# Kernel tuning notes

Hardware: AMD Instinct MI355X
Metric: run time of the kernel (lower is better)

Reference implementation:

```python
import jax, jax.numpy as jnp
import numpy as np

T, B, C, H, W = 4, 8, 256, 56, 56
HEADS = 8
D_NORM = 8.0
LAMDA = 1
CV = C * LAMDA
EPS = 1e-5


def quant_if(x, D):
    # Q_IFNode with Quant surrogate: integer spike counts clip(round(x),0,D),
    # straight-through gradient = 1 on [0, D].
    y = jnp.clip(jnp.round(x), 0.0, D)
    mask = ((x >= 0.0) & (x <= D)).astype(x.dtype)
    return x * mask + jax.lax.stop_gradient(y - x * mask)


def conv_bn(x, w, p):
    # 1x1 conv (pointwise channel mix) fused with eval-mode BatchNorm.
    # x: [T,B,Cin,H,W], w: [Cout,Cin], p: [4,Cout]=(gamma,beta,mean,var)
    y = jnp.einsum('oc,tbchw->tbohw', w, x)
    gamma, beta, mean, var = p[0], p[1], p[2], p[3]
    s = gamma / jnp.sqrt(var + EPS)
    return y * s[None, None, :, None, None] + (beta - mean * s)[None, None, :, None, None]


def _to_heads(t, c):
    # [T,B,c,H,W] -> [T,B,HEADS,N,c//HEADS]  (channel split h-outer, matches torch reshape)
    return t.reshape(T, B, HEADS, c // HEADS, H * W).transpose(0, 1, 2, 4, 3)


def setup_inputs():
    key = jax.random.key(0)
    ks = jax.random.split(key, 9)

    def bn_params(k, c):
        k1, k2, k3, k4 = jax.random.split(k, 4)
        return jnp.stack([
            jax.random.uniform(k1, (c,)) + 0.5,        # gamma
            jax.random.normal(k2, (c,)) * 0.1,          # beta
            jax.random.normal(k3, (c,)) * 0.1,          # running mean
            jax.random.uniform(k4, (c,)) + 0.5,         # running var
        ]).astype(jnp.float32)

    x = jax.random.normal(ks[0], (T, B, C, H, W), dtype=jnp.float32)
    w_scale = 1.0 / np.sqrt(C)
    return {
        'x': x,
        'qw': jax.random.normal(ks[1], (C, C), dtype=jnp.float32) * w_scale,
        'qbn': bn_params(ks[2], C),
        'kw': jax.random.normal(ks[3], (C, C), dtype=jnp.float32) * w_scale,
        'kbn': bn_params(ks[4], C),
        'vw': jax.random.normal(ks[5], (CV, C), dtype=jnp.float32) * w_scale,
        'vbn': bn_params(ks[6], CV),
        'pw': jax.random.normal(ks[7], (C, CV), dtype=jnp.float32) * w_scale,
        'pbn': bn_params(ks[8], C),
    }


def reference(x, qw, qbn, kw, kbn, vw, vbn, pw, pbn):
    dh = C // HEADS
    scale = dh ** (-0.5)

    xs = quant_if(x, D_NORM) / D_NORM                       # head_spike / D_Norm
    q = conv_bn(xs, qw, qbn)
    k = conv_bn(xs, kw, kbn)
    v = conv_bn(xs, vw, vbn)

    qh = _to_heads(quant_if(q, D_NORM) / D_NORM, C)         # [T,B,h,N,dh]
    kh = _to_heads(quant_if(k, D_NORM) / D_NORM, C)
    vh = _to_heads(quant_if(v, D_NORM) / D_NORM, CV)        # [T,B,h,N,dv]

    # Softmax-free linear attention: (q @ k^T) @ v == q @ (k^T @ v), O(N*d^2).
    kv = jnp.einsum('tbhnd,tbhne->tbhde', kh, vh)            # [T,B,h,dh,dv]
    o = jnp.einsum('tbhnd,tbhde->tbhne', qh, kv) * (scale * 2.0)

    # [T,B,h,N,dv] -> [T,B,CV,N]
    o = o.transpose(0, 1, 2, 4, 3).reshape(T, B, CV, H * W)
    o = quant_if(o, D_NORM) / D_NORM                         # attn_spike / D_Norm
    o = o.reshape(T, B, CV, H, W)
    out = conv_bn(o, pw, pbn)                                # [T,B,C,H,W]
    return out
```

## Files before the change

### kernel.cpp

```cpp
#include <hip/hip_runtime.h>
#include <stdint.h>

#define TB_ 32
#define C_ 256
#define N_ 3136
#define TBC (C_ * N_)
#define ACT_SZ (TB_ * TBC)
#define XSB_TB 819200
#define PARTS 7
#define CHUNK 448

typedef __attribute__((ext_vector_type(8))) short bf16x8;
typedef __attribute__((ext_vector_type(4))) float f32x4;

__device__ __forceinline__ void glds16(const void* gp, void* lp) {
  __builtin_amdgcn_global_load_lds(
      (const __attribute__((address_space(1))) unsigned int*)gp,
      (__attribute__((address_space(3))) unsigned int*)lp, 16, 0, 0);
}

__device__ __forceinline__ unsigned short bf16rn(float f, float* val) {
  unsigned b = __float_as_uint(f);
  unsigned r = (b + 0x7fffu + ((b >> 16) & 1u)) >> 16;
  *val = __uint_as_float(r << 16);
  return (unsigned short)r;
}

__device__ __forceinline__ int dot4u(unsigned a, unsigned b, int c) {
  c += (int)(a & 255u)         * (int)(b & 255u);
  c += (int)((a >> 8) & 255u)  * (int)((b >> 8) & 255u);
  c += (int)((a >> 16) & 255u) * (int)((b >> 16) & 255u);
  c += (int)(a >> 24)          * (int)(b >> 24);
  return c;
}

__device__ __forceinline__ int dot4(unsigned a, unsigned b, int c) {
#if defined(__has_builtin)
#if __has_builtin(__builtin_amdgcn_sdot4)
  return __builtin_amdgcn_sdot4((int)a, (int)b, c, false);
#else
  return dot4u(a, b, c);
#endif
#else
  return dot4u(a, b, c);
#endif
}

__global__ __launch_bounds__(256) void prep_all(
    const float* __restrict__ qbn, const float* __restrict__ kbn,
    const float* __restrict__ vbn, const float* __restrict__ pbn,
    const float* __restrict__ qw, const float* __restrict__ kw,
    const float* __restrict__ vw, const float* __restrict__ pw,
    float* __restrict__ bnw, unsigned short* __restrict__ wsp,
    int* __restrict__ kvg) {
  const int bx = blockIdx.x;
  const int t = threadIdx.x;
  if (bx == 0) {
    const float* ps[4] = {qbn, kbn, vbn, pbn};
#pragma unroll
    for (int i = 0; i < 4; ++i) {
      const float* p = ps[i];
      float g = p[t], be = p[256 + t], mn = p[512 + t], vr = p[768 + t];
      float s = g / sqrtf(vr + 1e-5f);
      float b = __fsub_rn(be, __fmul_rn(mn, s));
      bnw[i * 512 + t] = s;
      bnw[i * 512 + 256 + t] = b;
    }
  } else if (bx <= 1024) {
    const float* Ws[4] = {qw, kw, vw, pw};
    int id = bx - 1, co = id & 255, m = id >> 8;
    float w = Ws[m][co * 256 + t];
    float h1, h2, h3r;
    unsigned short u1 = bf16rn(w, &h1);
    float r1 = __fsub_rn(w, h1);
    unsigned short u2 = bf16rn(r1, &h2);
    float r2 = __fsub_rn(r1, h2);
    unsigned short u3 = bf16rn(r2, &h3r);
    int rt = co >> 7, ks = t >> 5;
    int lane = (co & 15) + 16 * ((t >> 3) & 3);
    unsigned short us[3] = {u1, u2, u3};
#pragma unroll
    for (int sp = 0; sp < 3; ++sp) {
      size_t off = (size_t)((((m * 3 + sp) * 2 + rt) * 8 + ks)) * 4096 + lane * 8 + (t & 7);
      wsp[off] = us[sp];
    }
  } else {
    int tb = bx - 1025;
    int4* p = (int4*)(kvg + (size_t)tb * 8192);
    for (int i = t; i < 2048; i += 256) p[i] = make_int4(0, 0, 0, 0);
  }
}

__global__ __launch_bounds__(256) void quant_x_t(const float* __restrict__ x,
                                                 unsigned short* __restrict__ xsb) {
  __shared__ unsigned short s[64 * 68];
  const int t = threadIdx.x;
  const int n0 = blockIdx.x * 64;
  const int tb = blockIdx.y;
  const float* X = x + (size_t)tb * TBC;
  const int nl = t & 63, cq = t >> 6;
  const int c16 = t >> 4, p4 = (t & 15) * 4;

  unsigned short* dstb = xsb + (size_t)tb * XSB_TB;
  for (int cb = 0; cb < 4; ++cb) {
    int cbase = cb * 64;
#pragma unroll
    for (int i = 0; i < 4; ++i) {
      int c = i * 16 + c16;
      float4 v = *(const float4*)&X[(size_t)(cbase + c) * N_ + n0 + p4];
      unsigned short r0 = (unsigned short)(__float_as_uint(fminf(fmaxf(rintf(v.x), 0.f), 8.f)) >> 16);
      unsigned short r1 = (unsigned short)(__float_as_uint(fminf(fmaxf(rintf(v.y), 0.f), 8.f)) >> 16);
      unsigned short r2 = (unsigned short)(__float_as_uint(fminf(fmaxf(rintf(v.z), 0.f), 8.f)) >> 16);
      unsigned short r3 = (unsigned short)(__float_as_uint(fminf(fmaxf(rintf(v.w), 0.f), 8.f)) >> 16);
      uint2 pk2;
      pk2.x = (unsigned)r0 | ((unsigned)r1 << 16);
      pk2.y = (unsigned)r2 | ((unsigned)r3 << 16);
      *(uint2*)&s[c * 68 + p4] = pk2;
    }
    __syncthreads();
#pragma unroll 2
    for (int j = 0; j < 2; ++j) {
      int ccl = j * 4 + cq;
      int cc = cb * 8 + ccl;
      unsigned short v8[8];
#pragma unroll
      for (int d = 0; d < 8; ++d) v8[d] = s[(ccl * 8 + d) * 68 + nl];
      int n = n0 + nl;
      uint4 pk;
      pk.x = (unsigned)v8[0] | ((unsigned)v8[1] << 16);
      pk.y = (unsigned)v8[2] | ((unsigned)v8[3] << 16);
      pk.z = (unsigned)v8[4] | ((unsigned)v8[5] << 16);
      pk.w = (unsigned)v8[6] | ((unsigned)v8[7] << 16);
      *(uint4*)&dstb[(size_t)(n >> 4) * 4096 + cc * 128 + (n & 15) * 8] = pk;
    }
    __syncthreads();
  }
}

__global__ __launch_bounds__(256) void qkv_mfma_sw(
    const unsigned short* __restrict__ xsb, const unsigned short* __restrict__ wsp,
    const float* __restrict__ bnw,
    uint8_t* __restrict__ qsb, uint8_t* __restrict__ ks_, uint8_t* __restrict__ vs) {
  __shared__ __align__(16) char smem[49152];
  const int t = threadIdx.x;
  const int L = t & 63, w = t >> 6;
  const int wrow = w >> 1, wcol = w & 1;
  const int b = blockIdx.x;
  const int oct = b / 48, rem = b % 48;
  const int s = rem >> 3, gl = rem & 7;
  const int g = oct * 8 + gl;
  const int ntile = g % 25, tb = g / 25;
  const int conv = s >> 1, rt = s & 1;
  const int n0 = ntile * 128;

  const char* Bb = (const char*)(xsb + (size_t)tb * XSB_TB) + (size_t)ntile * 65536;
  const char* Ab = (const char*)wsp + ((size_t)(conv * 3) * 16 + rt * 8) * 8192;

  f32x4 acc[4][4];
#pragma unroll
  for (int i = 0; i < 4; ++i)
#pragma unroll
    for (int j = 0; j < 4; ++j) acc[i][j] = (f32x4){0.f, 0.f, 0.f, 0.f};

  glds16(Ab + t * 16, smem + t * 16);
  glds16(Ab + t * 16 + 4096, smem + t * 16 + 4096);
  glds16(Bb + (size_t)w * 8192 + L * 16, smem + 8192 + t * 16);
  glds16(Bb + (size_t)(w + 4) * 8192 + L * 16, smem + 8192 + t * 16 + 4096);
  {
    char* slot1 = smem + 16384;
    const char* Ak1 = Ab + 8192;
    glds16(Ak1 + t * 16, slot1 + t * 16);
    glds16(Ak1 + t * 16 + 4096, slot1 + t * 16 + 4096);
    const char* Bk1 = Bb + 1024;
    glds16(Bk1 + (size_t)w * 8192 + L * 16, slot1 + 8192 + t * 16);
    glds16(Bk1 + (size_t)(w + 4) * 8192 + L * 16, slot1 + 8192 + t * 16 + 4096);
  }

#pragma unroll 1
  for (int st = 0; st < 24; ++st) {
    if (st < 23) {
      asm volatile("s_waitcnt vmcnt(4)" ::: "memory");
    } else {
      asm volatile("s_waitcnt vmcnt(0)" ::: "memory");
    }
    __builtin_amdgcn_s_barrier();
    const int s2 = st + 2;
    if (s2 < 24) {
      char* slotn = smem + (s2 % 3) * 16384;
      const char* Ak = Ab + (size_t)(((s2 >> 3) * 16) + (s2 & 7)) * 8192;
      glds16(Ak + t * 16, slotn + t * 16);
      glds16(Ak + t * 16 + 4096, slotn + t * 16 + 4096);
      const char* Bk = Bb + (size_t)(s2 & 7) * 1024;
      glds16(Bk + (size_t)w * 8192 + L * 16, slotn + 8192 + t * 16);
      glds16(Bk + (size_t)(w + 4) * 8192 + L * 16, slotn + 8192 + t * 16 + 4096);
    }
    char* slotc = smem + (st % 3) * 16384;
    bf16x8 af[4], bfr[4];
#pragma unroll
    for (int i = 0; i < 4; ++i) {
      af[i] = *(const bf16x8*)(slotc + (wrow * 4 + i) * 1024 + L * 16);
      bfr[i] = *(const bf16x8*)(slotc + 8192 + (wcol * 4 + i) * 1024 + L * 16);
    }
#pragma unroll
    for (int i = 0; i < 4; ++i)
#pragma unroll
      for (int j = 0; j < 4; ++j)
        acc[i][j] = __builtin_amdgcn_mfma_f32_16x16x32_bf16(af[i], bfr[j], acc[i][j], 0, 0, 0);
  }

  const float* sbn = bnw + conv * 512;
  const int rbase = rt * 128;
  if (conv == 0) {
    uint8_t* qtb = qsb + (size_t)tb * XSB_TB;
#pragma unroll
    for (int i = 0; i < 4; ++i) {
      int co0 = rbase + wrow * 64 + i * 16 + ((L >> 4) << 2);
      float s0 = sbn[co0], b0 = sbn[256 + co0];
      float s1 = sbn[co0 + 1], b1 = sbn[256 + co0 + 1];
      float s2v = sbn[co0 + 2], b2 = sbn[256 + co0 + 2];
      float s3 = sbn[co0 + 3], b3 = sbn[256 + co0 + 3];
#pragma unroll
      for (int j = 0; j < 4; ++j) {
        int n = n0 + wcol * 64 + j * 16 + (L & 15);
        if (n < N_) {
          float ss[4] = {s0, s1, s2v, s3}, bb[4] = {b0, b1, b2, b3};
          unsigned wb = 0;
#pragma unroll
          for (int r = 0; r < 4; ++r) {
            float y = acc[i][j][r] * 0.125f;
            float tt = __fadd_rn(__fmul_rn(y, ss[r]), bb[r]);
            float rr = fminf(fmaxf(rintf(tt), 0.f), 8.f);
            wb |= ((unsigned)(uint8_t)rr) << (8 * r);
          }
          *(unsigned*)&qtb[(size_t)(n >> 4) * 4096 + (co0 >> 3) * 128 + (n & 15) * 8 + (co0 & 7)] = wb;
        }
      }
    }
  } else {
    uint8_t* outp = (conv == 1 ? ks_ : vs) + (size_t)tb * TBC;
#pragma unroll
    for (int i = 0; i < 4; ++i) {
      int co0 = rbase + wrow * 64 + i * 16 + ((L >> 4) << 2);
#pragma unroll
      for (int j = 0; j < 4; ++j) {
        int n = n0 + wcol * 64 + j * 16 + (L & 15);
        if (n < N_) {
#pragma unroll
          for (int r = 0; r < 4; ++r) {
            int co = co0 + r;
            float y = acc[i][j][r] * 0.125f;
            float tt = __fadd_rn(__fmul_rn(y, sbn[co]), sbn[256 + co]);
            float rr = fminf(fmaxf(rintf(tt), 0.f), 8.f);
            outp[(size_t)co * N_ + n] = (uint8_t)rr;
          }
        }
      }
    }
  }
}

__global__ __launch_bounds__(256) void attn_kv(
    const uint8_t* __restrict__ ks, const uint8_t* __restrict__ vs,
    int* __restrict__ kvg) {
  const int h = blockIdx.x, tb = blockIdx.y, part = blockIdx.z;
  const int tid = threadIdx.x;
  __shared__ unsigned sk[32][68];
  __shared__ unsigned sv[32][68];
  const uint8_t* K = ks + (size_t)tb * TBC + h * 32 * N_;
  const uint8_t* V = vs + (size_t)tb * TBC + h * 32 * N_;
  const int d0 = (tid >> 4) * 2;
  const int e0 = (tid & 15) * 2;
  const int vsw = ((e0 >> 1) & 7) << 2;
  const int pbase = part * CHUNK;
  const int pend = pbase + CHUNK;
  int acc[2][2] = {};

  for (int nt = 0; nt < 2; ++nt) {
    int n0 = pbase + nt * 256;
    if (n0 >= pend) break;
    if (nt) __syncthreads();
#pragma unroll
    for (int i = 0; i < 8; ++i) {
      int idx = tid + i * 256;
      int d = idx >> 6, w2 = idx & 63;
      int n = n0 + w2 * 4;
      unsigned kw_ = 0, vw_ = 0;
      if (n < pend) {
        kw_ = *(const unsigned*)&K[d * N_ + n];
        vw_ = *(const unsigned*)&V[d * N_ + n];
      }
      sk[d][w2] = kw_;
      sv[d][w2 ^ (((d >> 1) & 7) << 2)] = vw_;
    }
    __syncthreads();
#pragma unroll
    for (int w2 = 0; w2 < 64; w2 += 4) {
      uint4 ka = *(const uint4*)&sk[d0][w2];
      uint4 kb = *(const uint4*)&sk[d0 + 1][w2];
      uint4 va = *(const uint4*)&sv[e0][w2 ^ vsw];
      uint4 vb = *(const uint4*)&sv[e0 + 1][w2 ^ vsw];
      unsigned kwds[2][4] = {{ka.x, ka.y, ka.z, ka.w}, {kb.x, kb.y, kb.z, kb.w}};
      unsigned vwds[2][4] = {{va.x, va.y, va.z, va.w}, {vb.x, vb.y, vb.z, vb.w}};
#pragma unroll
      for (int di = 0; di < 2; ++di)
#pragma unroll
        for (int ej = 0; ej < 2; ++ej)
#pragma unroll
          for (int c = 0; c < 4; ++c)
            acc[di][ej] = dot4(kwds[di][c], vwds[ej][c], acc[di][ej]);
    }
  }
  int* dst = kvg + ((size_t)(tb * 8 + h)) * 1024;
  atomicAdd(&dst[d0 * 32 + e0], acc[0][0]);
  atomicAdd(&dst[d0 * 32 + e0 + 1], acc[0][1]);
  atomicAdd(&dst[(d0 + 1) * 32 + e0], acc[1][0]);
  atomicAdd(&dst[(d0 + 1) * 32 + e0 + 1], acc[1][1]);
}

__global__ __launch_bounds__(256) void kv_finish(const int* __restrict__ kvg,
                                                 unsigned short* __restrict__ kvimg) {
  const int tb = blockIdx.x, t = threadIdx.x;
  const int* src = kvg + (size_t)tb * 8192;
  unsigned short* dst = kvimg + (size_t)tb * 24576;
#pragma unroll 4
  for (int i = 0; i < 32; ++i) {
    int idx = t + i * 256;
    int h = idx >> 10, rem = idx & 1023, d = rem >> 5, e = rem & 31;
    int v = src[idx];
    int b1 = (v > 0) ? (32 - __clz(v)) : 0;
    int sh1 = b1 > 8 ? b1 - 8 : 0;
    int hi = (v >> sh1) << sh1;
    int r1 = v - hi;
    int b2 = (r1 > 0) ? (32 - __clz(r1)) : 0;
    int sh2 = b2 > 8 ? b2 - 8 : 0;
    int mid = (r1 >> sh2) << sh2;
    int r2 = r1 - mid;
    int parts[3] = {hi, mid, r2};
    int mtile = e >> 4, lane = (e & 15) + 16 * (d >> 3), j = d & 7;
#pragma unroll
    for (int sp = 0; sp < 3; ++sp) {
      float f = (float)parts[sp];
      dst[(size_t)h * 3072 + (sp * 2 + mtile) * 512 + lane * 8 + j] =
          (unsigned short)(__float_as_uint(f) >> 16);
    }
  }
}

__global__ __launch_bounds__(256) void attn_o_mfma(
    const uint8_t* __restrict__ qsb, const unsigned short* __restrict__ kvimg,
    unsigned short* __restrict__ osb) {
  __shared__ __align__(16) char smem[28672];
  const int t = threadIdx.x;
  const int L = t & 63, wv = t >> 6;
  const int b = blockIdx.x;
  const int ntile = b % 25, tb = b / 25;
  const uint8_t* Q = qsb + (size_t)tb * XSB_TB + (size_t)ntile * 8 * 4096;
  const unsigned short* KV = kvimg + (size_t)tb * 24576;
  unsigned short* osb_tb = osb + (size_t)tb * XSB_TB;
  const float cscale = (float)(0.3535533905932738 / 512.0);

  const int gl2_[4] = {t >> 7, (t + 256) >> 7, (t + 512) >> 7, (t + 768) >> 7};
  {
    char* smB = smem;
    char* smA = smem + 8192;
    const char* Ah = (const char*)KV;
    glds16(Ah + t * 16, smA + t * 16);
    if (t < 128) glds16(Ah + 4096 + t * 16, smA + 4096 + t * 16);
#pragma unroll
    for (int it = 0; it < 4; ++it) {
      int w2 = t + it * 256;
      int gl2 = w2 >> 7, wl = w2 & 127, ccp = wl >> 5;
      int rem = (w2 * 4) & 127, n16 = rem >> 3, k7b = rem & 7;
      unsigned wd = *(const unsigned*)&Q[(size_t)gl2 * 4096 + (0 * 4 + ccp) * 128 + n16 * 8 + k7b];
      unsigned short* ds = (unsigned short*)smB + gl2 * 512 + (ccp * 16 + n16) * 8 + k7b;
      float f0 = (float)(wd & 255u), f1 = (float)((wd >> 8) & 255u);
      float f2 = (float)((wd >> 16) & 255u), f3 = (float)(wd >> 24);
      uint2 pk;
      pk.x = (__float_as_uint(f0) >> 16) | ((__float_as_uint(f1) >> 16) << 16);
      pk.y = (__float_as_uint(f2) >> 16) | ((__float_as_uint(f3) >> 16) << 16);
      *(uint2*)ds = pk;
    }
  }

#pragma unroll 1
  for (int h = 0; h < 8; ++h) {
    __syncthreads();
    char* cur = smem + (h & 1) * 14336;
    char* smB = cur;
    char* smA = cur + 8192;
    bf16x8 bfr[2];
#pragma unroll
    for (int jj = 0; jj < 2; ++jj)
      bfr[jj] = *(const bf16x8*)(smB + (wv * 2 + jj) * 1024 + L * 16);
    unsigned wd[4];
    if (h < 7) {
      char* alt = smem + ((h + 1) & 1) * 14336;
      const char* Ah = (const char*)(KV + (size_t)(h + 1) * 3072);
      glds16(Ah + t * 16, alt + 8192 + t * 16);
      if (t < 128) glds16(Ah + 4096 + t * 16, alt + 8192 + 4096 + t * 16);
#pragma unroll
      for (int it = 0; it < 4; ++it) {
        int w2 = t + it * 256;
        int gl2 = w2 >> 7, wl = w2 & 127, ccp = wl >> 5;
        int rem = (w2 * 4) & 127, n16 = rem >> 3, k7b = rem & 7;
        wd[it] = *(const unsigned*)&Q[(size_t)gl2 * 4096 + ((h + 1) * 4 + ccp) * 128 + n16 * 8 + k7b];
      }
    }
    f32x4 acc[2][2];
#pragma unroll
    for (int i = 0; i < 2; ++i)
#pragma unroll
      for (int jj = 0; jj < 2; ++jj) acc[i][jj] = (f32x4){0.f, 0.f, 0.f, 0.f};
#pragma unroll
    for (int sp = 0; sp < 3; ++sp) {
      bf16x8 a0 = *(const bf16x8*)(smA + (sp * 2 + 0) * 1024 + L * 16);
      bf16x8 a1 = *(const bf16x8*)(smA + (sp * 2 + 1) * 1024 + L * 16);
#pragma unroll
      for (int jj = 0; jj < 2; ++jj) {
        acc[0][jj] = __builtin_amdgcn_mfma_f32_16x16x32_bf16(a0, bfr[jj], acc[0][jj], 0, 0, 0);
        acc[1][jj] = __builtin_amdgcn_mfma_f32_16x16x32_bf16(a1, bfr[jj], acc[1][jj], 0, 0, 0);
      }
    }
    if (h < 7) {
      char* alt = smem + ((h + 1) & 1) * 14336;
#pragma unroll
      for (int it = 0; it < 4; ++it) {
        int w2 = t + it * 256;
        int gl2 = w2 >> 7, wl = w2 & 127, ccp = wl >> 5;
        int rem = (w2 * 4) & 127, n16 = rem >> 3, k7b = rem & 7;
        unsigned short* ds = (unsigned short*)alt + gl2 * 512 + (ccp * 16 + n16) * 8 + k7b;
        float f0 = (float)(wd[it] & 255u), f1 = (float)((wd[it] >> 8) & 255u);
        float f2 = (float)((wd[it] >> 16) & 255u), f3 = (float)(wd[it] >> 24);
        uint2 pk;
        pk.x = (__float_as_uint(f0) >> 16) | ((__float_as_uint(f1) >> 16) << 16);
        pk.y = (__float_as_uint(f2) >> 16) | ((__float_as_uint(f3) >> 16) << 16);
        *(uint2*)ds = pk;
      }
    }
#pragma unroll
    for (int i = 0; i < 2; ++i) {
      int c0 = h * 32 + i * 16 + ((L >> 4) << 2);
#pragma unroll
      for (int jj = 0; jj < 2; ++jj) {
        int n = ntile * 128 + (wv * 2 + jj) * 16 + (L & 15);
        if (n < N_) {
          unsigned short u[4];
#pragma unroll
          for (int r = 0; r < 4; ++r) {
            float of = acc[i][jj][r] * cscale;
            float rr = fminf(fmaxf(rintf(of), 0.f), 8.f);
            u[r] = (unsigned short)(__float_as_uint(rr) >> 16);
          }
          uint2 pk;
          pk.x = (unsigned)u[0] | ((unsigned)u[1] << 16);
          pk.y = (unsigned)u[2] | ((unsigned)u[3] << 16);
          *(uint2*)&osb_tb[(size_t)(n >> 4) * 4096 + (c0 >> 3) * 128 + (n & 15) * 8 + (c0 & 7)] = pk;
        }
      }
    }
  }
}

__global__ __launch_bounds__(256) void out_mfma_sw(
    const unsigned short* __restrict__ osb, const unsigned short* __restrict__ wsp,
    const float* __restrict__ bnw, float* __restrict__ out) {
  __shared__ __align__(16) char smem[49152];
  const int t = threadIdx.x;
  const int L = t & 63, w = t >> 6;
  const int wrow = w >> 1, wcol = w & 1;
  const int b = blockIdx.x;
  const int oct = b / 16, rem = b % 16;
  const int rt = rem >> 3, gl = rem & 7;
  const int g = oct * 8 + gl;
  const int ntile = g % 25, tb = g / 25;
  const int n0 = ntile * 128;
  const char* Bb = (const char*)(osb + (size_t)tb * XSB_TB) + (size_t)ntile * 65536;
  const char* Ab = (const char*)wsp + ((size_t)9 * 16 + rt * 8) * 8192;

  f32x4 acc[4][4];
#pragma unroll
  for (int i = 0; i < 4; ++i)
#pragma unroll
    for (int j = 0; j < 4; ++j) acc[i][j] = (f32x4){0.f, 0.f, 0.f, 0.f};

  glds16(Ab + t * 16, smem + t * 16);
  glds16(Ab + t * 16 + 4096, smem + t * 16 + 4096);
  glds16(Bb + (size_t)w * 8192 + L * 16, smem + 8192 + t * 16);
  glds16(Bb + (size_t)(w + 4) * 8192 + L * 16, smem + 8192 + t * 16 + 4096);
  {
    char* slot1 = smem + 16384;
    const char* Ak1 = Ab + 8192;
    glds16(Ak1 + t * 16, slot1 + t * 16);
    glds16(Ak1 + t * 16 + 4096, slot1 + t * 16 + 4096);
    const char* Bk1 = Bb + 1024;
    glds16(Bk1 + (size_t)w * 8192 + L * 16, slot1 + 8192 + t * 16);
    glds16(Bk1 + (size_t)(w + 4) * 8192 + L * 16, slot1 + 8192 + t * 16 + 4096);
  }

#pragma unroll 1
  for (int st = 0; st < 16; ++st) {
    if (st < 15) {
      asm volatile("s_waitcnt vmcnt(4)" ::: "memory");
    } else {
      asm volatile("s_waitcnt vmcnt(0)" ::: "memory");
    }
    __builtin_amdgcn_s_barrier();
    const int s2 = st + 2;
    if (s2 < 16) {
      char* slotn = smem + (s2 % 3) * 16384;
      const char* Ak = Ab + (size_t)(((s2 >> 3) * 16) + (s2 & 7)) * 8192;
      glds16(Ak + t * 16, slotn + t * 16);
      glds16(Ak + t * 16 + 4096, slotn + t * 16 + 4096);
      const char* Bk = Bb + (size_t)(s2 & 7) * 1024;
      glds16(Bk + (size_t)w * 8192 + L * 16, slotn + 8192 + t * 16);
      glds16(Bk + (size_t)(w + 4) * 8192 + L * 16, slotn + 8192 + t * 16 + 4096);
    }
    char* slotc = smem + (st % 3) * 16384;
    bf16x8 af[4], bfr[4];
#pragma unroll
    for (int i = 0; i < 4; ++i) {
      af[i] = *(const bf16x8*)(slotc + (wrow * 4 + i) * 1024 + L * 16);
      bfr[i] = *(const bf16x8*)(slotc + 8192 + (wcol * 4 + i) * 1024 + L * 16);
    }
#pragma unroll
    for (int i = 0; i < 4; ++i)
#pragma unroll
      for (int j = 0; j < 4; ++j)
        acc[i][j] = __builtin_amdgcn_mfma_f32_16x16x32_bf16(af[i], bfr[j], acc[i][j], 0, 0, 0);
  }

  float* O = out + (size_t)tb * TBC;
  const float* sbn = bnw + 3 * 512;
  const int rbase = rt * 128;
#pragma unroll
  for (int i = 0; i < 4; ++i) {
    int co0 = rbase + wrow * 64 + i * 16 + ((L >> 4) << 2);
#pragma unroll
    for (int j = 0; j < 4; ++j) {
      int n = n0 + wcol * 64 + j * 16 + (L & 15);
      if (n < N_) {
#pragma unroll
        for (int r = 0; r < 4; ++r) {
          int co = co0 + r;
          float y = acc[i][j][r] * 0.125f;
          O[(size_t)co * N_ + n] = __fadd_rn(__fmul_rn(y, sbn[co]), sbn[256 + co]);
        }
      }
    }
  }
}

extern "C" void kernel_launch(void* const* d_in, const int* in_sizes, int n_in,
                              void* d_out, int out_size, void* d_ws, size_t ws_size,
                              hipStream_t stream) {
  const float* x   = (const float*)d_in[0];
  const float* qw  = (const float*)d_in[1];
  const float* qbn = (const float*)d_in[2];
  const float* kw  = (const float*)d_in[3];
  const float* kbn = (const float*)d_in[4];
  const float* vw  = (const float*)d_in[5];
  const float* vbn = (const float*)d_in[6];
  const float* pw  = (const float*)d_in[7];
  const float* pbn = (const float*)d_in[8];
  float* out = (float*)d_out;

  uint8_t* ws = (uint8_t*)d_ws;
  float* bnw           = (float*)ws;
  unsigned short* wsp  = (unsigned short*)(ws + 8192);
  unsigned short* xsb  = (unsigned short*)(ws + 1581056);
  uint8_t* qsb         = ws + 54009856;
  uint8_t* ksp         = ws + 80224256;
  uint8_t* vsp         = ws + 105914368;
  int* kvg             = (int*)(ws + 131604480);
  unsigned short* kvimg = (unsigned short*)(ws + 132653056);
  unsigned short* osb  = xsb;

  prep_all<<<1057, 256, 0, stream>>>(qbn, kbn, vbn, pbn, qw, kw, vw, pw, bnw, wsp, kvg);
  quant_x_t<<<dim3(49, 32), 256, 0, stream>>>(x, xsb);
  qkv_mfma_sw<<<4800, 256, 0, stream>>>(xsb, wsp, bnw, qsb, ksp, vsp);
  attn_kv<<<dim3(8, 32, PARTS), 256, 0, stream>>>(ksp, vsp, kvg);
  kv_finish<<<32, 256, 0, stream>>>(kvg, kvimg);
  attn_o_mfma<<<800, 256, 0, stream>>>(qsb, kvimg, osb);
  out_mfma_sw<<<1600, 256, 0, stream>>>(osb, wsp, bnw, out);
}
```

Measured before the change: 395.8 us.

## Widen QKV GEMM N-tile to 160, switch to double buffering, parallelize kv_finish

The QKV MFMA kernel now uses 160-column N tiles, which gives 20 tiles covering 3136 columns exactly instead of 25 tiles of 128 with a ragged last tile. Each wave now computes a 4x5 fragment block. The pipeline changes from triple buffering with two stages in flight to double buffering with a full vmcnt(0) wait every step, and LDS use drops from 48 KB to 36 KB. kv_finish is split over 256 blocks instead of 32 to expose more parallelism. The wider tile cuts wasted padding work and repeated weight loads, but the shallower prefetch may expose more load latency.

```diff
diff --git a/kernel.cpp b/kernel.cpp
--- a/kernel.cpp
+++ b/kernel.cpp
@@ -141,7 +141,7 @@
     const unsigned short* __restrict__ xsb, const unsigned short* __restrict__ wsp,
     const float* __restrict__ bnw,
     uint8_t* __restrict__ qsb, uint8_t* __restrict__ ks_, uint8_t* __restrict__ vs) {
-  __shared__ __align__(16) char smem[49152];
+  __shared__ __align__(16) char smem[36864];
   const int t = threadIdx.x;
   const int L = t & 63, w = t >> 6;
   const int wrow = w >> 1, wcol = w & 1;
@@ -149,63 +149,54 @@
   const int oct = b / 48, rem = b % 48;
   const int s = rem >> 3, gl = rem & 7;
   const int g = oct * 8 + gl;
-  const int ntile = g % 25, tb = g / 25;
+  const int ntile = g % 20, tb = g / 20;
   const int conv = s >> 1, rt = s & 1;
-  const int n0 = ntile * 128;
-
-  const char* Bb = (const char*)(xsb + (size_t)tb * XSB_TB) + (size_t)ntile * 65536;
+  const int n0 = ntile * 160;
+
+  const char* Bb = (const char*)(xsb + (size_t)tb * XSB_TB) + (size_t)ntile * 81920;
   const char* Ab = (const char*)wsp + ((size_t)(conv * 3) * 16 + rt * 8) * 8192;
 
-  f32x4 acc[4][4];
+  f32x4 acc[4][5];
 #pragma unroll
   for (int i = 0; i < 4; ++i)
 #pragma unroll
-    for (int j = 0; j < 4; ++j) acc[i][j] = (f32x4){0.f, 0.f, 0.f, 0.f};
-
-  glds16(Ab + t * 16, smem + t * 16);
-  glds16(Ab + t * 16 + 4096, smem + t * 16 + 4096);
-  glds16(Bb + (size_t)w * 8192 + L * 16, smem + 8192 + t * 16);
-  glds16(Bb + (size_t)(w + 4) * 8192 + L * 16, smem + 8192 + t * 16 + 4096);
+    for (int j = 0; j < 5; ++j) acc[i][j] = (f32x4){0.f, 0.f, 0.f, 0.f};
+
   {
-    char* slot1 = smem + 16384;
-    const char* Ak1 = Ab + 8192;
-    glds16(Ak1 + t * 16, slot1 + t * 16);
-    glds16(Ak1 + t * 16 + 4096, slot1 + t * 16 + 4096);
-    const char* Bk1 = Bb + 1024;
-    glds16(Bk1 + (size_t)w * 8192 + L * 16, slot1 + 8192 + t * 16);
-    glds16(Bk1 + (size_t)(w + 4) * 8192 + L * 16, slot1 + 8192 + t * 16 + 4096);
+    glds16(Ab + t * 16, smem + t * 16);
+    glds16(Ab + t * 16 + 4096, smem + t * 16 + 4096);
+    glds16(Bb + (size_t)w * 8192 + L * 16, smem + 8192 + t * 16);
+    glds16(Bb + (size_t)(w + 4) * 8192 + L * 16, smem + 8192 + 4096 + t * 16);
+    if (w < 2) glds16(Bb + (size_t)(w + 8) * 8192 + L * 16, smem + 8192 + 8192 + t * 16);
   }
 
 #pragma unroll 1
   for (int st = 0; st < 24; ++st) {
-    if (st < 23) {
-      asm volatile("s_waitcnt vmcnt(4)" ::: "memory");
-    } else {
-      asm volatile("s_waitcnt vmcnt(0)" ::: "memory");
-    }
+    asm volatile("s_waitcnt vmcnt(0)" ::: "memory");
     __builtin_amdgcn_s_barrier();
-    const int s2 = st + 2;
-    if (s2 < 24) {
-      char* slotn = smem + (s2 % 3) * 16384;
-      const char* Ak = Ab + (size_t)(((s2 >> 3) * 16) + (s2 & 7)) * 8192;
+    const int s1 = st + 1;
+    if (s1 < 24) {
+      char* slotn = smem + (s1 & 1) * 18432;
+      const char* Ak = Ab + (size_t)(((s1 >> 3) * 16) + (s1 & 7)) * 8192;
       glds16(Ak + t * 16, slotn + t * 16);
       glds16(Ak + t * 16 + 4096, slotn + t * 16 + 4096);
-      const char* Bk = Bb + (size_t)(s2 & 7) * 1024;
+      const char* Bk = Bb + (size_t)(s1 & 7) * 1024;
       glds16(Bk + (size_t)w * 8192 + L * 16, slotn + 8192 + t * 16);
-      glds16(Bk + (size_t)(w + 4) * 8192 + L * 16, slotn + 8192 + t * 16 + 4096);
-    }
-    char* slotc = smem + (st % 3) * 16384;
-    bf16x8 af[4], bfr[4];
-#pragma unroll
-    for (int i = 0; i < 4; ++i) {
+      glds16(Bk + (size_t)(w + 4) * 8192 + L * 16, slotn + 8192 + 4096 + t * 16);
+      if (w < 2) glds16(Bk + (size_t)(w + 8) * 8192 + L * 16, slotn + 8192 + 8192 + t * 16);
+    }
+    char* slotc = smem + (st & 1) * 18432;
+    bf16x8 af[4];
+#pragma unroll
+    for (int i = 0; i < 4; ++i)
       af[i] = *(const bf16x8*)(slotc + (wrow * 4 + i) * 1024 + L * 16);
-      bfr[i] = *(const bf16x8*)(slotc + 8192 + (wcol * 4 + i) * 1024 + L * 16);
-    }
-#pragma unroll
-    for (int i = 0; i < 4; ++i)
-#pragma unroll
-      for (int j = 0; j < 4; ++j)
-        acc[i][j] = __builtin_amdgcn_mfma_f32_16x16x32_bf16(af[i], bfr[j], acc[i][j], 0, 0, 0);
+#pragma unroll
+    for (int j = 0; j < 5; ++j) {
+      bf16x8 bfr = *(const bf16x8*)(slotc + 8192 + (wcol * 5 + j) * 1024 + L * 16);
+#pragma unroll
+      for (int i = 0; i < 4; ++i)
+        acc[i][j] = __builtin_amdgcn_mfma_f32_16x16x32_bf16(af[i], bfr, acc[i][j], 0, 0, 0);
+    }
   }
 
   const float* sbn = bnw + conv * 512;
@@ -220,8 +211,8 @@
       float s2v = sbn[co0 + 2], b2 = sbn[256 + co0 + 2];
       float s3 = sbn[co0 + 3], b3 = sbn[256 + co0 + 3];
 #pragma unroll
-      for (int j = 0; j < 4; ++j) {
-        int n = n0 + wcol * 64 + j * 16 + (L & 15);
+      for (int j = 0; j < 5; ++j) {
+        int n = n0 + wcol * 80 + j * 16 + (L & 15);
         if (n < N_) {
           float ss[4] = {s0, s1, s2v, s3}, bb[4] = {b0, b1, b2, b3};
           unsigned wb = 0;
@@ -242,8 +233,8 @@
     for (int i = 0; i < 4; ++i) {
       int co0 = rbase + wrow * 64 + i * 16 + ((L >> 4) << 2);
 #pragma unroll
-      for (int j = 0; j < 4; ++j) {
-        int n = n0 + wcol * 64 + j * 16 + (L & 15);
+      for (int j = 0; j < 5; ++j) {
+        int n = n0 + wcol * 80 + j * 16 + (L & 15);
         if (n < N_) {
 #pragma unroll
           for (int r = 0; r < 4; ++r) {
@@ -319,12 +310,14 @@
 
 __global__ __launch_bounds__(256) void kv_finish(const int* __restrict__ kvg,
                                                  unsigned short* __restrict__ kvimg) {
-  const int tb = blockIdx.x, t = threadIdx.x;
+  const int bx = blockIdx.x, t = threadIdx.x;
+  const int tb = bx >> 3;
+  const int base = (bx & 7) * 1024;
   const int* src = kvg + (size_t)tb * 8192;
   unsigned short* dst = kvimg + (size_t)tb * 24576;
-#pragma unroll 4
-  for (int i = 0; i < 32; ++i) {
-    int idx = t + i * 256;
+#pragma unroll
+  for (int i = 0; i < 4; ++i) {
+    int idx = base + t + i * 256;
     int h = idx >> 10, rem = idx & 1023, d = rem >> 5, e = rem & 31;
     int v = src[idx];
     int b1 = (v > 0) ? (32 - __clz(v)) : 0;
@@ -359,7 +352,6 @@
   unsigned short* osb_tb = osb + (size_t)tb * XSB_TB;
   const float cscale = (float)(0.3535533905932738 / 512.0);
 
-  const int gl2_[4] = {t >> 7, (t + 256) >> 7, (t + 512) >> 7, (t + 768) >> 7};
   {
     char* smB = smem;
     char* smA = smem + 8192;
@@ -577,9 +569,9 @@
 
   prep_all<<<1057, 256, 0, stream>>>(qbn, kbn, vbn, pbn, qw, kw, vw, pw, bnw, wsp, kvg);
   quant_x_t<<<dim3(49, 32), 256, 0, stream>>>(x, xsb);
-  qkv_mfma_sw<<<4800, 256, 0, stream>>>(xsb, wsp, bnw, qsb, ksp, vsp);
+  qkv_mfma_sw<<<3840, 256, 0, stream>>>(xsb, wsp, bnw, qsb, ksp, vsp);
   attn_kv<<<dim3(8, 32, PARTS), 256, 0, stream>>>(ksp, vsp, kvg);
-  kv_finish<<<32, 256, 0, stream>>>(kvg, kvimg);
+  kv_finish<<<256, 256, 0, stream>>>(kvg, kvimg);
   attn_o_mfma<<<800, 256, 0, stream>>>(qsb, kvimg, osb);
   out_mfma_sw<<<1600, 256, 0, stream>>>(osb, wsp, bnw, out);
 }
```

After: 403.2 us. About the same (+1.9%).
